# Performance work log

Measured on AMD Instinct MI355X. Metric: run time of the kernel, lower is better.

## Reference

```python
import jax, jax.numpy as jnp
import numpy as np

H = 64      # LSTM hidden units
OUT = 10    # dense softmax classes


def setup_inputs() -> dict:
    key = jax.random.key(0)
    k0, k1, k2, k3 = jax.random.split(key, 4)
    B, T, D = 256, 1024, 128
    x = jax.random.normal(k0, (B, T, D), dtype=jnp.float32)
    # small weight scale keeps relu cell state stable over 1024 steps
    W = jax.random.normal(k1, (D, 4 * H), dtype=jnp.float32) * 0.05
    U = jax.random.normal(k2, (H, 4 * H), dtype=jnp.float32) * 0.05
    b = jnp.zeros((4 * H,), jnp.float32)
    Wd = jax.random.normal(k3, (H, OUT), dtype=jnp.float32) * 0.05
    bd = jnp.zeros((OUT,), jnp.float32)
    return {"x": x, "W": W, "U": U, "b": b, "Wd": Wd, "bd": bd}


def hard_sigmoid(z):
    # legacy Keras recurrent_activation default
    return jnp.clip(0.2 * z + 0.5, 0.0, 1.0)


def lstm_last_hidden(x, W, U, b):
    # x: [B,T,D] -> last hidden state [B,H]
    B = x.shape[0]
    xw = jnp.einsum('btd,dg->btg', x, W) + b  # [B,T,4H] input projection, computed once

    def step(carry, xt):
        h, c = carry
        z = xt + h @ U  # [B,4H]
        i = hard_sigmoid(z[:, :H])
        f = hard_sigmoid(z[:, H:2 * H])
        g = jax.nn.relu(z[:, 2 * H:3 * H])   # activation='relu' (candidate)
        o = hard_sigmoid(z[:, 3 * H:])
        c = f * c + i * g
        h = o * jax.nn.relu(c)               # activation='relu' on cell output
        return (h, c), None

    h0 = jnp.zeros((B, H), x.dtype)
    (h, _), _ = jax.lax.scan(step, (h0, h0), jnp.swapaxes(xw, 0, 1))
    return h


def reference(x, W, U, b, Wd, bd):
    h = lstm_last_hidden(x, W, U, b)          # [B,H]
    return jax.nn.softmax(h @ Wd + bd, axis=-1)  # [B,OUT]
```

## Files before the change

kernel.cpp:

```cpp
#include <hip/hip_runtime.h>
#include <hip/hip_bf16.h>

#define Hh   64
#define G4   256
#define Dd   128
#define Bsz  256
#define Tt   1024
#define NOUT 10

typedef __bf16  bf16x8 __attribute__((ext_vector_type(8)));
typedef __bf16  bf16x4 __attribute__((ext_vector_type(4)));
typedef float   f32x4v __attribute__((ext_vector_type(4)));

__device__ __forceinline__ int rho_origcol(int rho) {
    const int g  = rho >> 6;
    const int s  = (rho >> 5) & 1;
    const int d2 = (rho >> 4) & 1;
    const int kq = (rho >> 2) & 3;
    const int dl = rho & 3;
    return g * 64 + (32 * s + 8 * kq + 4 * d2 + dl);
}


__device__ __forceinline__ void gld_lds16(const void* g, void* l) {
    __builtin_amdgcn_global_load_lds(
        (const __attribute__((address_space(1))) unsigned int*)g,
        (__attribute__((address_space(3))) unsigned int*)l, 16, 0, 0);
}

__global__ __launch_bounds__(128)
void k0_prep(const float* __restrict__ W, const float* __restrict__ b,
             __bf16* __restrict__ Wt, float* __restrict__ bias2) {
    const int rho = blockIdx.x;
    const int k   = threadIdx.x;
    const int col = rho_origcol(rho);
    const bool isg = ((rho >> 6) == 2);
    const float sc = isg ? 1.f : 0.2f;
    Wt[(size_t)rho * Dd + k] = (__bf16)(sc * W[(size_t)k * G4 + col]);
    if (k == 0) bias2[rho] = sc * b[col] + (isg ? 0.f : 0.5f);
}

#define K1_RT 8

__global__ __launch_bounds__(256)
void k1_mfma(const float* __restrict__ x, const __bf16* __restrict__ Wt,
             const float* __restrict__ bias, __bf16* __restrict__ xw) {
    const int tid = threadIdx.x;
    const int w   = tid >> 6;
    const int l   = tid & 63;
    const int r16 = l & 15;
    const int kq  = l >> 4;
    const size_t rowbase = (size_t)blockIdx.x * (16 * K1_RT);

    bf16x8 bfr[4][4];
    float  bval[4];
#pragma unroll
    for (int ct = 0; ct < 4; ++ct) {
        const int col = w * 64 + ct * 16 + r16;
        const __bf16* wp = Wt + (size_t)col * Dd + kq * 8;
#pragma unroll
        for (int kk = 0; kk < 4; ++kk)
            bfr[ct][kk] = *(const bf16x8*)(wp + kk * 32);
        bval[ct] = bias[col];
    }

    for (int rt = 0; rt < K1_RT; ++rt) {
        const size_t arow = rowbase + rt * 16 + r16;
        const float* xr = x + arow * Dd + kq * 8;
        bf16x8 afr[4];
#pragma unroll
        for (int kk = 0; kk < 4; ++kk) {
            const float4 lo = *(const float4*)(xr + kk * 32);
            const float4 hi = *(const float4*)(xr + kk * 32 + 4);
            afr[kk][0] = (__bf16)lo.x; afr[kk][1] = (__bf16)lo.y;
            afr[kk][2] = (__bf16)lo.z; afr[kk][3] = (__bf16)lo.w;
            afr[kk][4] = (__bf16)hi.x; afr[kk][5] = (__bf16)hi.y;
            afr[kk][6] = (__bf16)hi.z; afr[kk][7] = (__bf16)hi.w;
        }
        f32x4v acc[4];
#pragma unroll
        for (int ct = 0; ct < 4; ++ct)
            acc[ct] = (f32x4v){bval[ct], bval[ct], bval[ct], bval[ct]};
#pragma unroll
        for (int ct = 0; ct < 4; ++ct)
#pragma unroll
            for (int kk = 0; kk < 4; ++kk)
                acc[ct] = __builtin_amdgcn_mfma_f32_16x16x32_bf16(
                              afr[kk], bfr[ct][kk], acc[ct], 0, 0, 0);

        const size_t orow0 = rowbase + rt * 16 + kq * 4;
#pragma unroll
        for (int ct = 0; ct < 4; ++ct) {
            const int col = w * 64 + ct * 16 + r16;
#pragma unroll
            for (int rr = 0; rr < 4; ++rr)
                xw[(orow0 + rr) * G4 + col] = (__bf16)acc[ct][rr];
        }
    }
}

#define SST 8

__global__ __launch_bounds__(256, 1)
void k2_scan(const __bf16* __restrict__ xw, const float* __restrict__ U,
             float* __restrict__ hout) {
    const int tid = threadIdx.x;
    const int w   = tid >> 6;
    const int l   = tid & 63;
    const int kq  = l >> 4;
    const int m   = l & 15;
    const int s_  = w >> 1, d2 = w & 1;
    const int G   = blockIdx.x;

    __shared__ __align__(16) unsigned char ring[2][SST][8192];
    __shared__ __align__(16) __bf16 hx[2][16][72];

    bf16x8 au[4][2];
#pragma unroll
    for (int g = 0; g < 4; ++g) {
        const float sc = (g == 2) ? 1.f : 0.2f;
        const int col = rho_origcol(64 * g + 16 * w + m);
#pragma unroll
        for (int ks = 0; ks < 2; ++ks)
#pragma unroll
            for (int j = 0; j < 8; ++j)
                au[g][ks][j] = (__bf16)(sc * U[(size_t)(ks * 32 + kq * 8 + j) * G4 + col]);
    }

    float c4[4]  = {0.f, 0.f, 0.f, 0.f};
    float hv4[4] = {0.f, 0.f, 0.f, 0.f};

    {
        const bf16x4 z4 = {(__bf16)0.f, (__bf16)0.f, (__bf16)0.f, (__bf16)0.f};
        *(bf16x4*)&hx[1][m][32 * s_ + 8 * kq + 4 * d2] = z4;
    }

    const char* xwc = (const char*)xw;
    const char* src_j[2];
#pragma unroll
    for (int j = 0; j < 2; ++j) {
        const int i  = 2 * w + j;
        const int mp = 2 * i + (l >> 5);
        const int sch = ((l & 31) - mp) & 31;
        src_j[j] = xwc + (size_t)(16 * G + mp) * 524288 + (size_t)sch * 16;
    }
    int rd_off[4];
#pragma unroll
    for (int g = 0; g < 4; ++g)
        rd_off[g] = m * 512 + (((8 * g + 2 * w + (kq >> 1) + m) & 31) << 4)
                    + ((kq & 1) << 3);

#pragma unroll
    for (int buf = 0; buf < 2; ++buf)
#pragma unroll
        for (int stp = 0; stp < SST; ++stp)
#pragma unroll
            for (int j = 0; j < 2; ++j)
                gld_lds16(src_j[j] + (size_t)(buf * SST + stp) * 512,
                          &ring[buf][stp][(2 * w + j) * 1024]);
    __syncthreads();

    uint2  dz[4];
    f32x4v accN[4];
    bf16x8 bh0, bh1;

    for (int S = 0; S < Tt / SST; ++S) {
        const int cur = S & 1;

        asm volatile("s_waitcnt vmcnt(16)" ::: "memory");
        __builtin_amdgcn_sched_barrier(0);
        __builtin_amdgcn_s_barrier();
        __builtin_amdgcn_sched_barrier(0);

#pragma unroll
        for (int g = 0; g < 4; ++g)
            dz[g] = *(const uint2*)&ring[cur][0][rd_off[g]];
#pragma unroll
        for (int g = 0; g < 4; ++g) {
            accN[g][0] = __builtin_bit_cast(float, dz[g].x << 16);
            accN[g][1] = __builtin_bit_cast(float, dz[g].x & 0xFFFF0000u);
            accN[g][2] = __builtin_bit_cast(float, dz[g].y << 16);
            accN[g][3] = __builtin_bit_cast(float, dz[g].y & 0xFFFF0000u);
        }

#pragma unroll
        for (int stp = 0; stp < SST; ++stp) {
            const int rp = (stp + 1) & 1;

            bh0 = *(const bf16x8*)&hx[rp][m][8 * kq];
            bh1 = *(const bf16x8*)&hx[rp][m][32 + 8 * kq];

            f32x4v acc[4];
#pragma unroll
            for (int g = 0; g < 4; ++g) {
                acc[g] = __builtin_amdgcn_mfma_f32_16x16x32_bf16(au[g][0], bh0, accN[g], 0, 0, 0);
                acc[g] = __builtin_amdgcn_mfma_f32_16x16x32_bf16(au[g][1], bh1, acc[g], 0, 0, 0);
            }

            bf16x4 hb;
#pragma unroll
            for (int r = 0; r < 4; ++r) {
                const float gi = __builtin_amdgcn_fmed3f(acc[0][r], 0.f, 1.f);
                const float gf = __builtin_amdgcn_fmed3f(acc[1][r], 0.f, 1.f);
                const float gg = fmaxf(acc[2][r], 0.f);
                const float go = __builtin_amdgcn_fmed3f(acc[3][r], 0.f, 1.f);
                c4[r] = fmaf(gf, c4[r], gi * gg);
                hv4[r] = go * fmaxf(c4[r], 0.f);
                hb[r] = (__bf16)hv4[r];
            }

            *(bf16x4*)&hx[stp & 1][m][32 * s_ + 8 * kq + 4 * d2] = hb;

            if (stp < SST - 1) {
#pragma unroll
                for (int g = 0; g < 4; ++g)
                    dz[g] = *(const uint2*)&ring[cur][stp + 1][rd_off[g]];
                asm volatile("s_waitcnt lgkmcnt(4)" ::: "memory");
            } else {
                asm volatile("s_waitcnt lgkmcnt(0)" ::: "memory");
            }
            __builtin_amdgcn_sched_barrier(0);
            __builtin_amdgcn_s_barrier();
            __builtin_amdgcn_sched_barrier(0);

            if (stp < SST - 1) {
#pragma unroll
                for (int g = 0; g < 4; ++g) {
                    accN[g][0] = __builtin_bit_cast(float, dz[g].x << 16);
                    accN[g][1] = __builtin_bit_cast(float, dz[g].x & 0xFFFF0000u);
                    accN[g][2] = __builtin_bit_cast(float, dz[g].y << 16);
                    accN[g][3] = __builtin_bit_cast(float, dz[g].y & 0xFFFF0000u);
                }
            }
        }

        {
            int tn0 = (S + 2) * SST;
            if (tn0 > Tt - SST) tn0 = Tt - SST;
#pragma unroll
            for (int stp = 0; stp < SST; ++stp)
#pragma unroll
                for (int j = 0; j < 2; ++j)
                    gld_lds16(src_j[j] + (size_t)(tn0 + stp) * 512,
                              &ring[cur][stp][(2 * w + j) * 1024]);
        }
    }

#pragma unroll
    for (int r = 0; r < 4; ++r)
        hout[(size_t)(G * 16 + m) * Hh + 32 * s_ + 8 * kq + 4 * d2 + r] = hv4[r];
}

__global__ __launch_bounds__(256)
void k3_dense(const float* __restrict__ hin, const float* __restrict__ Wd,
              const float* __restrict__ bd, float* __restrict__ out) {
    __shared__ float wd[Hh * NOUT];
    __shared__ float bds[NOUT];
    for (int i = threadIdx.x; i < Hh * NOUT; i += blockDim.x) wd[i] = Wd[i];
    if (threadIdx.x < NOUT) bds[threadIdx.x] = bd[threadIdx.x];
    __syncthreads();

    const int r = threadIdx.x;
    if (r < Bsz) {
        float hrow[Hh];
#pragma unroll
        for (int j = 0; j < Hh; ++j) hrow[j] = hin[(size_t)r * Hh + j];
        float logits[NOUT];
#pragma unroll
        for (int o = 0; o < NOUT; ++o) {
            float acc = bds[o];
#pragma unroll
            for (int j = 0; j < Hh; ++j) acc = fmaf(hrow[j], wd[j * NOUT + o], acc);
            logits[o] = acc;
        }
        float mx = logits[0];
#pragma unroll
        for (int o = 1; o < NOUT; ++o) mx = fmaxf(mx, logits[o]);
        float s = 0.f;
#pragma unroll
        for (int o = 0; o < NOUT; ++o) { logits[o] = expf(logits[o] - mx); s += logits[o]; }
        const float inv = 1.f / s;
#pragma unroll
        for (int o = 0; o < NOUT; ++o) out[(size_t)r * NOUT + o] = logits[o] * inv;
    }
}

extern "C" void kernel_launch(void* const* d_in, const int* in_sizes, int n_in,
                              void* d_out, int out_size, void* d_ws, size_t ws_size,
                              hipStream_t stream) {
    const float* x  = (const float*)d_in[0];
    const float* W  = (const float*)d_in[1];
    const float* U  = (const float*)d_in[2];
    const float* b  = (const float*)d_in[3];
    const float* Wd = (const float*)d_in[4];
    const float* bd = (const float*)d_in[5];
    float* out = (float*)d_out;

    const size_t xw_bytes = (size_t)Bsz * Tt * G4 * sizeof(__bf16);
    __bf16* xw    = (__bf16*)d_ws;
    float*  hbuf  = (float*)((char*)d_ws + xw_bytes);
    __bf16* Wt    = (__bf16*)((char*)hbuf + (size_t)Bsz * Hh * sizeof(float));
    float*  bias2 = (float*)((char*)Wt + (size_t)G4 * Dd * sizeof(__bf16));

    k0_prep<<<G4, Dd, 0, stream>>>(W, b, Wt, bias2);
    k1_mfma<<<(Bsz * Tt) / (16 * K1_RT), 256, 0, stream>>>(x, Wt, bias2, xw);
    k2_scan<<<Bsz / 16, 256, 0, stream>>>(xw, U, hbuf);
    k3_dense<<<1, 256, 0, stream>>>(hbuf, Wd, bd, out);
}
```

Measured before the change: 547.8 us.

## Interleave two independent batch groups per scan block to hide recurrence latency

Each k2_scan block now carries two independent 16-row batch groups, so the grid shrinks from 16 to 8 blocks. The groups' MFMA, gate math, LDS ring buffers and h exchange buffers are interleaved within every timestep. The aim is to fill the latency of the serial MFMA-to-activation-to-LDS dependency chain with independent work and to spread each per-step barrier over twice the useful work. To keep LDS use the same, the prefetch stage depth drops from 8 to 4 steps. That means more frequent global refills and more register pressure from the doubled accumulators.

```diff
diff --git a/kernel.cpp b/kernel.cpp
--- a/kernel.cpp
+++ b/kernel.cpp
@@ -99,7 +99,7 @@
     }
 }
 
-#define SST 8
+#define SST 4
 
 __global__ __launch_bounds__(256, 1)
 void k2_scan(const __bf16* __restrict__ xw, const float* __restrict__ U,
@@ -110,10 +110,10 @@
     const int kq  = l >> 4;
     const int m   = l & 15;
     const int s_  = w >> 1, d2 = w & 1;
-    const int G   = blockIdx.x;
-
-    __shared__ __align__(16) unsigned char ring[2][SST][8192];
-    __shared__ __align__(16) __bf16 hx[2][16][72];
+    const int G0  = blockIdx.x * 2;
+
+    __shared__ __align__(16) unsigned char ring[2][2][SST][8192];
+    __shared__ __align__(16) __bf16 hx[2][2][16][72];
 
     bf16x8 au[4][2];
 #pragma unroll
@@ -127,23 +127,31 @@
                 au[g][ks][j] = (__bf16)(sc * U[(size_t)(ks * 32 + kq * 8 + j) * G4 + col]);
     }
 
-    float c4[4]  = {0.f, 0.f, 0.f, 0.f};
-    float hv4[4] = {0.f, 0.f, 0.f, 0.f};
+    float c4[2][4], hv4[2][4];
+#pragma unroll
+    for (int g2 = 0; g2 < 2; ++g2)
+#pragma unroll
+        for (int r = 0; r < 4; ++r) { c4[g2][r] = 0.f; hv4[g2][r] = 0.f; }
 
     {
         const bf16x4 z4 = {(__bf16)0.f, (__bf16)0.f, (__bf16)0.f, (__bf16)0.f};
-        *(bf16x4*)&hx[1][m][32 * s_ + 8 * kq + 4 * d2] = z4;
+#pragma unroll
+        for (int g2 = 0; g2 < 2; ++g2)
+            *(bf16x4*)&hx[g2][1][m][32 * s_ + 8 * kq + 4 * d2] = z4;
     }
 
     const char* xwc = (const char*)xw;
-    const char* src_j[2];
-#pragma unroll
-    for (int j = 0; j < 2; ++j) {
-        const int i  = 2 * w + j;
-        const int mp = 2 * i + (l >> 5);
-        const int sch = ((l & 31) - mp) & 31;
-        src_j[j] = xwc + (size_t)(16 * G + mp) * 524288 + (size_t)sch * 16;
-    }
+    const char* srcp[2][2];
+#pragma unroll
+    for (int g2 = 0; g2 < 2; ++g2)
+#pragma unroll
+        for (int j = 0; j < 2; ++j) {
+            const int i  = 2 * w + j;
+            const int mp = 2 * i + (l >> 5);
+            const int sch = ((l & 31) - mp) & 31;
+            srcp[g2][j] = xwc + (size_t)(16 * (G0 + g2) + mp) * 524288
+                          + (size_t)sch * 16;
+        }
     int rd_off[4];
 #pragma unroll
     for (int g = 0; g < 4; ++g)
@@ -153,16 +161,18 @@
 #pragma unroll
     for (int buf = 0; buf < 2; ++buf)
 #pragma unroll
-        for (int stp = 0; stp < SST; ++stp)
-#pragma unroll
-            for (int j = 0; j < 2; ++j)
-                gld_lds16(src_j[j] + (size_t)(buf * SST + stp) * 512,
-                          &ring[buf][stp][(2 * w + j) * 1024]);
+        for (int g2 = 0; g2 < 2; ++g2)
+#pragma unroll
+            for (int stp = 0; stp < SST; ++stp)
+#pragma unroll
+                for (int j = 0; j < 2; ++j)
+                    gld_lds16(srcp[g2][j] + (size_t)(buf * SST + stp) * 512,
+                              &ring[g2][buf][stp][(2 * w + j) * 1024]);
     __syncthreads();
 
-    uint2  dz[4];
-    f32x4v accN[4];
-    bf16x8 bh0, bh1;
+    uint2  dz[2][4];
+    f32x4v accN[2][4];
+    bf16x8 bh0[2], bh1[2];
 
     for (int S = 0; S < Tt / SST; ++S) {
         const int cur = S & 1;
@@ -173,49 +183,66 @@
         __builtin_amdgcn_sched_barrier(0);
 
 #pragma unroll
-        for (int g = 0; g < 4; ++g)
-            dz[g] = *(const uint2*)&ring[cur][0][rd_off[g]];
-#pragma unroll
-        for (int g = 0; g < 4; ++g) {
-            accN[g][0] = __builtin_bit_cast(float, dz[g].x << 16);
-            accN[g][1] = __builtin_bit_cast(float, dz[g].x & 0xFFFF0000u);
-            accN[g][2] = __builtin_bit_cast(float, dz[g].y << 16);
-            accN[g][3] = __builtin_bit_cast(float, dz[g].y & 0xFFFF0000u);
-        }
+        for (int g2 = 0; g2 < 2; ++g2)
+#pragma unroll
+            for (int g = 0; g < 4; ++g)
+                dz[g2][g] = *(const uint2*)&ring[g2][cur][0][rd_off[g]];
+#pragma unroll
+        for (int g2 = 0; g2 < 2; ++g2)
+#pragma unroll
+            for (int g = 0; g < 4; ++g) {
+                accN[g2][g][0] = __builtin_bit_cast(float, dz[g2][g].x << 16);
+                accN[g2][g][1] = __builtin_bit_cast(float, dz[g2][g].x & 0xFFFF0000u);
+                accN[g2][g][2] = __builtin_bit_cast(float, dz[g2][g].y << 16);
+                accN[g2][g][3] = __builtin_bit_cast(float, dz[g2][g].y & 0xFFFF0000u);
+            }
 
 #pragma unroll
         for (int stp = 0; stp < SST; ++stp) {
             const int rp = (stp + 1) & 1;
 
-            bh0 = *(const bf16x8*)&hx[rp][m][8 * kq];
-            bh1 = *(const bf16x8*)&hx[rp][m][32 + 8 * kq];
-
-            f32x4v acc[4];
-#pragma unroll
-            for (int g = 0; g < 4; ++g) {
-                acc[g] = __builtin_amdgcn_mfma_f32_16x16x32_bf16(au[g][0], bh0, accN[g], 0, 0, 0);
-                acc[g] = __builtin_amdgcn_mfma_f32_16x16x32_bf16(au[g][1], bh1, acc[g], 0, 0, 0);
-            }
-
-            bf16x4 hb;
-#pragma unroll
-            for (int r = 0; r < 4; ++r) {
-                const float gi = __builtin_amdgcn_fmed3f(acc[0][r], 0.f, 1.f);
-                const float gf = __builtin_amdgcn_fmed3f(acc[1][r], 0.f, 1.f);
-                const float gg = fmaxf(acc[2][r], 0.f);
-                const float go = __builtin_amdgcn_fmed3f(acc[3][r], 0.f, 1.f);
-                c4[r] = fmaf(gf, c4[r], gi * gg);
-                hv4[r] = go * fmaxf(c4[r], 0.f);
-                hb[r] = (__bf16)hv4[r];
-            }
-
-            *(bf16x4*)&hx[stp & 1][m][32 * s_ + 8 * kq + 4 * d2] = hb;
+#pragma unroll
+            for (int g2 = 0; g2 < 2; ++g2) {
+                bh0[g2] = *(const bf16x8*)&hx[g2][rp][m][8 * kq];
+                bh1[g2] = *(const bf16x8*)&hx[g2][rp][m][32 + 8 * kq];
+            }
+
+            f32x4v acc[2][4];
+#pragma unroll
+            for (int g2 = 0; g2 < 2; ++g2)
+#pragma unroll
+                for (int g = 0; g < 4; ++g) {
+                    acc[g2][g] = __builtin_amdgcn_mfma_f32_16x16x32_bf16(
+                                     au[g][0], bh0[g2], accN[g2][g], 0, 0, 0);
+                    acc[g2][g] = __builtin_amdgcn_mfma_f32_16x16x32_bf16(
+                                     au[g][1], bh1[g2], acc[g2][g], 0, 0, 0);
+                }
+
+#pragma unroll
+            for (int g2 = 0; g2 < 2; ++g2) {
+                bf16x4 hb;
+#pragma unroll
+                for (int r = 0; r < 4; ++r) {
+                    const float gi = __builtin_amdgcn_fmed3f(acc[g2][0][r], 0.f, 1.f);
+                    const float gf = __builtin_amdgcn_fmed3f(acc[g2][1][r], 0.f, 1.f);
+                    const float gg = fmaxf(acc[g2][2][r], 0.f);
+                    const float go = __builtin_amdgcn_fmed3f(acc[g2][3][r], 0.f, 1.f);
+                    c4[g2][r] = fmaf(gf, c4[g2][r], gi * gg);
+                    hv4[g2][r] = go * fmaxf(c4[g2][r], 0.f);
+                    hb[r] = (__bf16)hv4[g2][r];
+                }
+                *(bf16x4*)&hx[g2][stp & 1][m][32 * s_ + 8 * kq + 4 * d2] = hb;
+            }
+
+            __builtin_amdgcn_sched_barrier(0);
 
             if (stp < SST - 1) {
 #pragma unroll
-                for (int g = 0; g < 4; ++g)
-                    dz[g] = *(const uint2*)&ring[cur][stp + 1][rd_off[g]];
-                asm volatile("s_waitcnt lgkmcnt(4)" ::: "memory");
+                for (int g2 = 0; g2 < 2; ++g2)
+#pragma unroll
+                    for (int g = 0; g < 4; ++g)
+                        dz[g2][g] = *(const uint2*)&ring[g2][cur][stp + 1][rd_off[g]];
+                asm volatile("s_waitcnt lgkmcnt(8)" ::: "memory");
             } else {
                 asm volatile("s_waitcnt lgkmcnt(0)" ::: "memory");
             }
@@ -225,12 +252,14 @@
 
             if (stp < SST - 1) {
 #pragma unroll
-                for (int g = 0; g < 4; ++g) {
-                    accN[g][0] = __builtin_bit_cast(float, dz[g].x << 16);
-                    accN[g][1] = __builtin_bit_cast(float, dz[g].x & 0xFFFF0000u);
-                    accN[g][2] = __builtin_bit_cast(float, dz[g].y << 16);
-                    accN[g][3] = __builtin_bit_cast(float, dz[g].y & 0xFFFF0000u);
-                }
+                for (int g2 = 0; g2 < 2; ++g2)
+#pragma unroll
+                    for (int g = 0; g < 4; ++g) {
+                        accN[g2][g][0] = __builtin_bit_cast(float, dz[g2][g].x << 16);
+                        accN[g2][g][1] = __builtin_bit_cast(float, dz[g2][g].x & 0xFFFF0000u);
+                        accN[g2][g][2] = __builtin_bit_cast(float, dz[g2][g].y << 16);
+                        accN[g2][g][3] = __builtin_bit_cast(float, dz[g2][g].y & 0xFFFF0000u);
+                    }
             }
         }
 
@@ -238,17 +267,22 @@
             int tn0 = (S + 2) * SST;
             if (tn0 > Tt - SST) tn0 = Tt - SST;
 #pragma unroll
-            for (int stp = 0; stp < SST; ++stp)
-#pragma unroll
-                for (int j = 0; j < 2; ++j)
-                    gld_lds16(src_j[j] + (size_t)(tn0 + stp) * 512,
-                              &ring[cur][stp][(2 * w + j) * 1024]);
-        }
-    }
-
-#pragma unroll
-    for (int r = 0; r < 4; ++r)
-        hout[(size_t)(G * 16 + m) * Hh + 32 * s_ + 8 * kq + 4 * d2 + r] = hv4[r];
+            for (int g2 = 0; g2 < 2; ++g2)
+#pragma unroll
+                for (int stp = 0; stp < SST; ++stp)
+#pragma unroll
+                    for (int j = 0; j < 2; ++j)
+                        gld_lds16(srcp[g2][j] + (size_t)(tn0 + stp) * 512,
+                                  &ring[g2][cur][stp][(2 * w + j) * 1024]);
+        }
+    }
+
+#pragma unroll
+    for (int g2 = 0; g2 < 2; ++g2)
+#pragma unroll
+        for (int r = 0; r < 4; ++r)
+            hout[(size_t)((G0 + g2) * 16 + m) * Hh + 32 * s_ + 8 * kq + 4 * d2 + r]
+                = hv4[g2][r];
 }
 
 __global__ __launch_bounds__(256)
@@ -304,6 +338,6 @@
 
     k0_prep<<<G4, Dd, 0, stream>>>(W, b, Wt, bias2);
     k1_mfma<<<(Bsz * Tt) / (16 * K1_RT), 256, 0, stream>>>(x, Wt, bias2, xw);
-    k2_scan<<<Bsz / 16, 256, 0, stream>>>(xw, U, hbuf);
+    k2_scan<<<Bsz / 32, 256, 0, stream>>>(xw, U, hbuf);
     k3_dense<<<1, 256, 0, stream>>>(hbuf, Wd, bd, out);
 }
```

New measurement: 856.3 us. 1.56x slower.
